# Kernel optimization log

Hardware: AMD Instinct MI355X
Metric: run time of the kernel (lower is better)

The kernel has to match this reference:

```python
import jax, jax.numpy as jnp
import numpy as np

N, E, IN, HID, H, G, CLS = 20000, 160000, 128, 96, 6, 512, 128
HD = H * HID  # heads * out_channels = 576
ARC_S = 30.0  # ArcFace scale (no margin at inference, no labels passed)


def _lin_params(key, fan_in, fan_out):
    k1, k2 = jax.random.split(key)
    lim = 1.0 / np.sqrt(fan_in)
    W = jax.random.uniform(k1, (fan_in, fan_out), minval=-lim, maxval=lim, dtype=jnp.float32)
    b = jax.random.uniform(k2, (fan_out,), minval=-lim, maxval=lim, dtype=jnp.float32)
    return W, b


def setup_inputs() -> dict:
    key = jax.random.key(0)
    ks = jax.random.split(key, 32)
    x = jax.random.normal(ks[0], (N, IN), dtype=jnp.float32)
    edge_index = jax.random.randint(ks[1], (2, E), 0, N, dtype=jnp.int64)
    batch = jnp.sort(jax.random.randint(ks[2], (N,), 0, G, dtype=jnp.int64))
    # conv1: IN -> HID (per-head dim HID, H heads)
    Wq1, bq1 = _lin_params(ks[3], IN, HD)
    Wk1, bk1 = _lin_params(ks[4], IN, HD)
    Wv1, bv1 = _lin_params(ks[5], IN, HD)
    Ws1, bs1 = _lin_params(ks[6], IN, HID)
    # convs 2..5 share shapes: HID -> HID, stacked on leading axis of 4
    def stack(fn_keys, fi, fo):
        Ws, bs = zip(*[_lin_params(k, fi, fo) for k in fn_keys])
        return jnp.stack(Ws), jnp.stack(bs)
    Wq_r, bq_r = stack(ks[7:11], HID, HD)
    Wk_r, bk_r = stack(ks[11:15], HID, HD)
    Wv_r, bv_r = stack(ks[15:19], HID, HD)
    Ws_r, bs_r = stack(ks[19:23], HID, HID)
    fc1_w, fc1_b = _lin_params(ks[23], HID, HID)
    fc2_w, fc2_b = _lin_params(ks[24], HID, HID)
    arc_w = jax.random.normal(ks[25], (CLS, HID), dtype=jnp.float32)
    return dict(x=x, edge_index=edge_index, batch=batch,
                Wq1=Wq1, bq1=bq1, Wk1=Wk1, bk1=bk1, Wv1=Wv1, bv1=bv1, Ws1=Ws1, bs1=bs1,
                Wq_r=Wq_r, bq_r=bq_r, Wk_r=Wk_r, bk_r=bk_r, Wv_r=Wv_r, bv_r=bv_r,
                Ws_r=Ws_r, bs_r=bs_r,
                fc1_w=fc1_w, fc1_b=fc1_b, fc2_w=fc2_w, fc2_b=fc2_b, arc_w=arc_w)


def transformer_conv(x, src, dst, Wq, bq, Wk, bk, Wv, bv, Ws, bs):
    n = x.shape[0]
    q = (x @ Wq + bq).reshape(n, H, HID)
    k = (x @ Wk + bk).reshape(n, H, HID)
    v = (x @ Wv + bv).reshape(n, H, HID)
    # edge-wise attention logits [E, H]
    alpha = jnp.einsum('ehd,ehd->eh', q[dst], k[src]) / jnp.sqrt(jnp.float32(HID))
    # segment softmax over incoming edges of each destination node
    m = jax.ops.segment_max(alpha, dst, num_segments=n)
    a = jnp.exp(alpha - m[dst])
    s = jax.ops.segment_sum(a, dst, num_segments=n)
    a = a / s[dst]
    out = jax.ops.segment_sum(a[:, :, None] * v[src], dst, num_segments=n)  # [n, H, HID]
    # concat=False -> mean over heads; root_weight skip connection
    return out.mean(axis=1) + x @ Ws + bs


def reference(x, edge_index, batch,
              Wq1, bq1, Wk1, bk1, Wv1, bv1, Ws1, bs1,
              Wq_r, bq_r, Wk_r, bk_r, Wv_r, bv_r, Ws_r, bs_r,
              fc1_w, fc1_b, fc2_w, fc2_b, arc_w):
    src, dst = edge_index[0], edge_index[1]
    h = jax.nn.relu(transformer_conv(x, src, dst, Wq1, bq1, Wk1, bk1, Wv1, bv1, Ws1, bs1))
    for i in range(4):  # gtconv2..gtconv5
        h = jax.nn.relu(transformer_conv(h, src, dst, Wq_r[i], bq_r[i], Wk_r[i], bk_r[i],
                                         Wv_r[i], bv_r[i], Ws_r[i], bs_r[i]))
    # global mean pool over graphs
    sums = jax.ops.segment_sum(h, batch, num_segments=G)
    cnt = jax.ops.segment_sum(jnp.ones((h.shape[0], 1), h.dtype), batch, num_segments=G)
    g = sums / jnp.maximum(cnt, 1.0)
    g = jax.nn.relu(g @ fc1_w + fc1_b)
    g = jax.nn.relu(g @ fc2_w + fc2_b)
    # ArcFace without labels: scaled cosine logits
    gn = g / (jnp.linalg.norm(g, axis=-1, keepdims=True) + 1e-12)
    wn = arc_w / (jnp.linalg.norm(arc_w, axis=-1, keepdims=True) + 1e-12)
    return ARC_S * (gn @ wn.T)
```

## Files before the change

### kernel.cpp

```cpp
#include <hip/hip_runtime.h>
#include <math.h>

#define N_NODES 20000
#define N_EDGES 160000
#define DIM_IN  128
#define HIDDEN  96
#define NH      6
#define HD      576
#define LDROW   704
#define KVF8LD  1152
#define NALL    1824
#define NGRAPH  512
#define NCLS    128
#define CHUNK   32
#define SLD     104
#define BSTR    112

typedef unsigned short ushort_t;
typedef unsigned char uchar_t;
typedef __attribute__((ext_vector_type(8))) short bf16x8;
typedef __attribute__((ext_vector_type(4))) float f32x4;
typedef __attribute__((ext_vector_type(2))) float f32x2;

static __device__ __forceinline__ ushort_t f2bf(float f) {
    unsigned int u = __float_as_uint(f);
    return (ushort_t)((u + 0x7fffu + ((u >> 16) & 1u)) >> 16);
}
static __device__ __forceinline__ float bfs(ushort_t u) { return __uint_as_float((unsigned int)u << 16); }
static __device__ __forceinline__ float bflo(unsigned int u) { return __uint_as_float(u << 16); }
static __device__ __forceinline__ float bfhi(unsigned int u) { return __uint_as_float(u & 0xffff0000u); }

#define PREP_CVT_BLOCKS 10000
#define PREP_DEG_BLOCKS 625
#define PREP_GB_BLOCKS  3
__global__ void k_prep(const float* __restrict__ x, ushort_t* __restrict__ xb,
                       const int* __restrict__ edst, int* __restrict__ deg,
                       const int* __restrict__ batch, int* __restrict__ gbound)
{
    int b = blockIdx.x;
    if (b < PREP_CVT_BLOCKS) {
        int i = b * 256 + threadIdx.x;
        if (i < N_NODES * DIM_IN) xb[i] = f2bf(x[i]);
    } else if (b < PREP_CVT_BLOCKS + PREP_DEG_BLOCKS) {
        int e = (b - PREP_CVT_BLOCKS) * 256 + threadIdx.x;
        if (e < N_EDGES) atomicAdd(&deg[edst[e]], 1);
    } else {
        int g = (b - PREP_CVT_BLOCKS - PREP_DEG_BLOCKS) * 256 + threadIdx.x;
        if (g <= NGRAPH) {
            int lo = 0, hi = N_NODES;
            while (lo < hi) {
                int mid = (lo + hi) >> 1;
                if (batch[mid] < g) lo = mid + 1; else hi = mid;
            }
            gbound[g] = lo;
        }
    }
}

__global__ void k_cvt_wT_all(
    const float* __restrict__ Wq1, const float* __restrict__ Wk1,
    const float* __restrict__ Wv1, const float* __restrict__ Ws1,
    const float* __restrict__ Wq_r, const float* __restrict__ Wk_r,
    const float* __restrict__ Wv_r, const float* __restrict__ Ws_r,
    ushort_t* __restrict__ Wb0, ushort_t* __restrict__ Wbr)
{
    const int L = blockIdx.y;
    const int K = (L == 0) ? DIM_IN : HIDDEN;
    int i = blockIdx.x * blockDim.x + threadIdx.x;
    if (i >= K * NALL) return;
    const float *Wq, *Wk, *Wv, *Ws; ushort_t* dst;
    if (L == 0) { Wq = Wq1; Wk = Wk1; Wv = Wv1; Ws = Ws1; dst = Wb0; }
    else {
        int j = L - 1;
        Wq = Wq_r + (size_t)j * HIDDEN * HD; Wk = Wk_r + (size_t)j * HIDDEN * HD;
        Wv = Wv_r + (size_t)j * HIDDEN * HD; Ws = Ws_r + (size_t)j * HIDDEN * HIDDEN;
        dst = Wbr + (size_t)j * HIDDEN * NALL;
    }
    int n = i / K, k = i - n * K;
    float v;
    if (n < 576)       v = Wq[(size_t)k * HD + n];
    else if (n < 1152) v = Wk[(size_t)k * HD + (n - 576)];
    else if (n < 1728) v = Wv[(size_t)k * HD + (n - 1152)];
    else               v = Ws[(size_t)k * HIDDEN + (n - 1728)];
    dst[i] = f2bf(v);
}

template<int KDIM>
__global__ __launch_bounds__(256) void gemm_qkvs_mfma(
    const ushort_t* __restrict__ A, int M,
    const ushort_t* __restrict__ WbT,
    const float* __restrict__ bq, const float* __restrict__ bk,
    const float* __restrict__ bv, const float* __restrict__ bs,
    ushort_t* __restrict__ kvqs, uchar_t* __restrict__ kvf8)
{
    constexpr int LDB = KDIM + 8;
    constexpr int K8  = KDIM >> 3;
    __shared__ __align__(16) ushort_t smem[128 * SLD];
    const int t    = threadIdx.x;
    const int lane = t & 63;
    const int w    = t >> 6;
    const int wm   = w & 1, wn = w >> 1;
    const int quad = lane >> 4;
    const int l16  = lane & 15;
    const int m0   = blockIdx.y * 128;
    const int rb   = blockIdx.x;
    const int n0   = rb * 96;

    for (int idx = t; idx < 96 * K8; idx += 256) {
        int c = idx / K8, kc = idx - c * K8;
        uint4 v = *(const uint4*)(WbT + (size_t)(n0 + c) * KDIM + kc * 8);
        *(uint4*)(&smem[c * LDB + kc * 8]) = v;
    }

    const ushort_t* Arow[4];
    #pragma unroll
    for (int i = 0; i < 4; i++) {
        int row = m0 + wm * 64 + i * 16 + l16;
        row = min(row, M - 1);
        Arow[i] = A + (size_t)row * KDIM + quad * 8;
    }
    __syncthreads();

    f32x4 acc[4][3] = {};
    #pragma unroll
    for (int ks = 0; ks < KDIM; ks += 32) {
        bf16x8 af[4], bfv[3];
        #pragma unroll
        for (int i = 0; i < 4; i++) af[i] = *(const bf16x8*)(Arow[i] + ks);
        #pragma unroll
        for (int j = 0; j < 3; j++)
            bfv[j] = *(const bf16x8*)(&smem[(wn * 48 + j * 16 + l16) * LDB + ks + quad * 8]);
        #pragma unroll
        for (int i = 0; i < 4; i++)
            #pragma unroll
            for (int j = 0; j < 3; j++)
                acc[i][j] = __builtin_amdgcn_mfma_f32_16x16x32_bf16(af[i], bfv[j], acc[i][j], 0, 0, 0);
    }

    int region; const float* biasp;
    if (rb < 6)       { region = 0; biasp = bq; }
    else if (rb < 12) { region = 1; biasp = bk; }
    else if (rb < 18) { region = 2; biasp = bv; }
    else              { region = 3; biasp = bs; }
    const int colbase = (region == 3) ? 0 : (rb - region * 6) * 96;
    float bj[3];
    #pragma unroll
    for (int j = 0; j < 3; j++) bj[j] = biasp[colbase + wn * 48 + j * 16 + l16];

    __syncthreads();

    if (region == 1 || region == 2) {
        uchar_t* bstage = (uchar_t*)smem;
        #pragma unroll
        for (int i = 0; i < 4; i++) {
            #pragma unroll
            for (int r = 0; r < 4; r++) {
                int row = wm * 64 + i * 16 + quad * 4 + r;
                #pragma unroll
                for (int j = 0; j < 3; j++) {
                    float v = acc[i][j][r] + bj[j];
                    int pk = __builtin_amdgcn_cvt_pk_fp8_f32(v, v, 0, false);
                    bstage[row * BSTR + wn * 48 + j * 16 + l16] = (uchar_t)(pk & 0xff);
                }
            }
        }
        __syncthreads();
        const int c0 = (rb - 6) * 96;
        for (int idx = t; idx < 128 * 6; idx += 256) {
            int r = idx / 6, v4 = idx - r * 6;
            int row = m0 + r;
            if (row < M)
                *(uint4*)(kvf8 + (size_t)row * KVF8LD + c0 + v4 * 16) =
                    *(const uint4*)(bstage + r * BSTR + v4 * 16);
        }
    } else {
        int dstoff = (region == 0) ? n0 : 576;
        #pragma unroll
        for (int i = 0; i < 4; i++) {
            #pragma unroll
            for (int r = 0; r < 4; r++) {
                int row = wm * 64 + i * 16 + quad * 4 + r;
                #pragma unroll
                for (int j = 0; j < 3; j++)
                    smem[row * SLD + wn * 48 + j * 16 + l16] = f2bf(acc[i][j][r] + bj[j]);
            }
        }
        __syncthreads();
        for (int idx = t; idx < 128 * 12; idx += 256) {
            int r = idx / 12, v = idx - r * 12;
            int row = m0 + r;
            if (row < M)
                *(uint4*)(kvqs + (size_t)row * LDROW + dstoff + v * 8) =
                    *(const uint4*)(&smem[r * SLD + v * 8]);
        }
    }
}

__global__ __launch_bounds__(1024) void k_scan(const int* __restrict__ deg,
                                               int* __restrict__ row_ptr,
                                               int* __restrict__ cursor)
{
    __shared__ int part[1024];
    int t = threadIdx.x;
    const int chunk = (N_NODES + 1023) / 1024;
    int b = t * chunk;
    int s = 0;
    for (int i = 0; i < chunk; i++)
        if (b + i < N_NODES) s += deg[b + i];
    part[t] = s;
    __syncthreads();
    for (int o = 1; o < 1024; o <<= 1) {
        int v = (t >= o) ? part[t - o] : 0;
        __syncthreads();
        part[t] += v;
        __syncthreads();
    }
    int run = part[t] - s;
    for (int i = 0; i < chunk; i++) {
        if (b + i < N_NODES) {
            row_ptr[b + i] = run;
            cursor[b + i]  = run;
            run += deg[b + i];
        }
    }
    if (t == 1023) row_ptr[N_NODES] = part[1023];
}

__global__ void k_scatter(const int* __restrict__ esrc, const int* __restrict__ edst,
                          int* __restrict__ cursor, int* __restrict__ csrc)
{
    int e = blockIdx.x * blockDim.x + threadIdx.x;
    if (e < N_EDGES) {
        int pos = atomicAdd(&cursor[edst[e]], 1);
        csrc[pos] = esrc[e];
    }
}

__global__ __launch_bounds__(64) void node_attn(
    const ushort_t* __restrict__ kvqs, const uchar_t* __restrict__ kvf8,
    const int* __restrict__ row_ptr, const int* __restrict__ csrc,
    ushort_t* __restrict__ hb)
{
    const int n    = blockIdx.x;
    const int lane = threadIdx.x;

    __shared__ float QA[HD];
    __shared__ float wbuf[CHUNK * NH];
    __shared__ int   srcs[CHUNK];
    __shared__ float mh[NH], lh[NH], scl[NH], linv[NH];

    const int beg = row_ptr[n], end = row_ptr[n + 1];
    const ushort_t* qk = kvqs + (size_t)n * LDROW;

    {
        uint4 v = *(const uint4*)(qk + lane * 8);
        unsigned int uu[4] = {v.x, v.y, v.z, v.w};
        #pragma unroll
        for (int j = 0; j < 4; j++) {
            QA[lane * 8 + 2 * j]     = bflo(uu[j]);
            QA[lane * 8 + 2 * j + 1] = bfhi(uu[j]);
        }
        if (lane < 8) {
            uint4 v2 = *(const uint4*)(qk + (64 + lane) * 8);
            unsigned int uu2[4] = {v2.x, v2.y, v2.z, v2.w};
            #pragma unroll
            for (int j = 0; j < 4; j++) {
                QA[(64 + lane) * 8 + 2 * j]     = bflo(uu2[j]);
                QA[(64 + lane) * 8 + 2 * j + 1] = bfhi(uu2[j]);
            }
        }
    }
    if (lane < NH) { mh[lane] = -1e30f; lh[lane] = 0.f; }

    const int sub = lane >> 5;
    const int h32 = lane & 31;
    const int g   = h32 >> 2;
    const int gg  = (g < 6) ? g : 0;
    const int qr  = h32 & 3;
    const int hh  = lane >> 3;
    const int j8  = lane & 7;
    const uchar_t* vb = kvf8 + 576 + ((hh < 6) ? hh : 0) * HIDDEN + j8 * 12;

    float acc[12];
    #pragma unroll
    for (int d = 0; d < 12; d++) acc[d] = 0.f;
    const float qa = 0.10206207261596577f;

    __syncthreads();

    for (int cb = beg; cb < end; cb += CHUNK) {
        const int c = min(CHUNK, end - cb);
        if (lane < c) srcs[lane] = csrc[cb + lane];
        __syncthreads();

        for (int eb = 0; eb < c; eb += 8) {
            unsigned int kb[4][6];
            #pragma unroll
            for (int j = 0; j < 4; j++) {
                int e = eb + 2 * j + sub;
                int src = srcs[(e < c) ? e : 0];
                const uchar_t* kp = kvf8 + (size_t)src * KVF8LD + gg * HIDDEN + qr * 24;
                uint2 a0 = *(const uint2*)(kp);
                uint2 a1 = *(const uint2*)(kp + 8);
                uint2 a2 = *(const uint2*)(kp + 16);
                kb[j][0] = a0.x; kb[j][1] = a0.y;
                kb[j][2] = a1.x; kb[j][3] = a1.y;
                kb[j][4] = a2.x; kb[j][5] = a2.y;
            }
            const float* qb = &QA[gg * HIDDEN + qr * 24];
            #pragma unroll
            for (int j = 0; j < 4; j++) {
                int e = eb + 2 * j + sub;
                bool act = (e < c) && (g < 6);
                float p = 0.f;
                #pragma unroll
                for (int k2 = 0; k2 < 6; k2++) {
                    f32x2 lo = __builtin_amdgcn_cvt_pk_f32_fp8(kb[j][k2], false);
                    f32x2 hi = __builtin_amdgcn_cvt_pk_f32_fp8(kb[j][k2], true);
                    p += lo[0] * qb[4 * k2]     + lo[1] * qb[4 * k2 + 1]
                       + hi[0] * qb[4 * k2 + 2] + hi[1] * qb[4 * k2 + 3];
                }
                p += __shfl_xor(p, 1, 64);
                p += __shfl_xor(p, 2, 64);
                if (act && qr == 0) wbuf[e * NH + g] = p * qa;
            }
        }
        __syncthreads();

        #pragma unroll
        for (int s = 0; s < 3; s++) {
            int h = 2 * s + sub;
            float logit = (h32 < c) ? wbuf[h32 * NH + h] : -1e30f;
            float cm = logit;
            #pragma unroll
            for (int o = 16; o; o >>= 1) cm = fmaxf(cm, __shfl_xor(cm, o, 32));
            cm = fmaxf(cm, mh[h]);
            float wv = (h32 < c) ? __expf(logit - cm) : 0.f;
            if (h32 < c) wbuf[h32 * NH + h] = wv;
            float lp = wv;
            #pragma unroll
            for (int o = 16; o; o >>= 1) lp += __shfl_xor(lp, o, 32);
            if (h32 == 0) {
                float sc = __expf(mh[h] - cm);
                scl[h] = sc;
                lh[h] = lh[h] * sc + lp;
                mh[h] = cm;
            }
        }
        __syncthreads();

        if (lane < 48) {
            float sc = scl[hh];
            #pragma unroll
            for (int d = 0; d < 12; d++) acc[d] *= sc;
            int e = 0;
            for (; e + 4 <= c; e += 4) {
                unsigned int r[4][3];
                #pragma unroll
                for (int j = 0; j < 4; j++) {
                    const uchar_t* p = vb + (size_t)srcs[e + j] * KVF8LD;
                    r[j][0] = *(const unsigned int*)(p);
                    r[j][1] = *(const unsigned int*)(p + 4);
                    r[j][2] = *(const unsigned int*)(p + 8);
                }
                #pragma unroll
                for (int j = 0; j < 4; j++) {
                    float w0 = wbuf[(e + j) * NH + hh];
                    #pragma unroll
                    for (int k = 0; k < 3; k++) {
                        f32x2 lo = __builtin_amdgcn_cvt_pk_f32_fp8(r[j][k], false);
                        f32x2 hi = __builtin_amdgcn_cvt_pk_f32_fp8(r[j][k], true);
                        acc[4 * k]     += w0 * lo[0];
                        acc[4 * k + 1] += w0 * lo[1];
                        acc[4 * k + 2] += w0 * hi[0];
                        acc[4 * k + 3] += w0 * hi[1];
                    }
                }
            }
            for (; e < c; e++) {
                const uchar_t* p0 = vb + (size_t)srcs[e] * KVF8LD;
                float w0 = wbuf[e * NH + hh];
                #pragma unroll
                for (int k = 0; k < 3; k++) {
                    unsigned int r = *(const unsigned int*)(p0 + 4 * k);
                    f32x2 lo = __builtin_amdgcn_cvt_pk_f32_fp8(r, false);
                    f32x2 hi = __builtin_amdgcn_cvt_pk_f32_fp8(r, true);
                    acc[4 * k]     += w0 * lo[0];
                    acc[4 * k + 1] += w0 * lo[1];
                    acc[4 * k + 2] += w0 * hi[0];
                    acc[4 * k + 3] += w0 * hi[1];
                }
            }
        }
        __syncthreads();
    }

    if (lane < NH) linv[lane] = (lh[lane] > 0.f) ? 1.0f / lh[lane] : 0.f;
    __syncthreads();
    if (lane < 48) {
        float li = linv[hh];
        #pragma unroll
        for (int d = 0; d < 12; d++)
            QA[hh * HIDDEN + j8 * 12 + d] = acc[d] * li;
    }
    __syncthreads();

    {
        int d = lane;
        float s = (QA[d] + QA[HIDDEN + d] + QA[2 * HIDDEN + d] +
                   QA[3 * HIDDEN + d] + QA[4 * HIDDEN + d] + QA[5 * HIDDEN + d])
                  * (1.0f / 6.0f);
        s += bfs(qk[576 + d]);
        s = fmaxf(s, 0.0f);
        hb[n * HIDDEN + d] = f2bf(s);
        if (lane < 32) {
            int d2 = 64 + lane;
            float s2 = (QA[d2] + QA[HIDDEN + d2] + QA[2 * HIDDEN + d2] +
                        QA[3 * HIDDEN + d2] + QA[4 * HIDDEN + d2] + QA[5 * HIDDEN + d2])
                       * (1.0f / 6.0f);
            s2 += bfs(qk[576 + d2]);
            s2 = fmaxf(s2, 0.0f);
            hb[n * HIDDEN + d2] = f2bf(s2);
        }
    }
}

__global__ __launch_bounds__(128) void k_head(
    const ushort_t* __restrict__ hb, const int* __restrict__ gbound,
    const float* __restrict__ fc1w, const float* __restrict__ fc1b,
    const float* __restrict__ fc2w, const float* __restrict__ fc2b,
    const float* __restrict__ arcw, float* __restrict__ out)
{
    int g = blockIdx.x, t = threadIdx.x;
    __shared__ float v0[HIDDEN], v1[HIDDEN], v2[HIDDEN];
    __shared__ float gnorm;
    const int s0 = gbound[g], s1 = gbound[g + 1];
    float cnt = fmaxf((float)(s1 - s0), 1.0f);
    if (t < HIDDEN) {
        float s = 0.f;
        for (int n = s0; n < s1; n++) s += bfs(hb[(size_t)n * HIDDEN + t]);
        v0[t] = s / cnt;
    }
    __syncthreads();
    if (t < HIDDEN) {
        float s = fc1b[t];
        for (int k = 0; k < HIDDEN; k++) s += v0[k] * fc1w[k * HIDDEN + t];
        v1[t] = fmaxf(s, 0.f);
    }
    __syncthreads();
    if (t < HIDDEN) {
        float s = fc2b[t];
        for (int k = 0; k < HIDDEN; k++) s += v1[k] * fc2w[k * HIDDEN + t];
        v2[t] = fmaxf(s, 0.f);
    }
    __syncthreads();
    if (t == 0) {
        float s = 0.f;
        for (int k = 0; k < HIDDEN; k++) s += v2[k] * v2[k];
        gnorm = sqrtf(s) + 1e-12f;
    }
    __syncthreads();
    if (t < NCLS) {
        float dot = 0.f, wn = 0.f;
        const float* wr = arcw + (size_t)t * HIDDEN;
        for (int k = 0; k < HIDDEN; k++) {
            float w = wr[k];
            dot += w * v2[k];
            wn  += w * w;
        }
        out[g * NCLS + t] = 30.0f * dot / (gnorm * (sqrtf(wn) + 1e-12f));
    }
}

extern "C" void kernel_launch(void* const* d_in, const int* in_sizes, int n_in,
                              void* d_out, int out_size, void* d_ws, size_t ws_size,
                              hipStream_t stream)
{
    (void)in_sizes; (void)n_in; (void)out_size; (void)ws_size;

    const float* x     = (const float*)d_in[0];
    const int*   ei    = (const int*)d_in[1];
    const int*   batch = (const int*)d_in[2];
    const float* Wq1 = (const float*)d_in[3];  const float* bq1 = (const float*)d_in[4];
    const float* Wk1 = (const float*)d_in[5];  const float* bk1 = (const float*)d_in[6];
    const float* Wv1 = (const float*)d_in[7];  const float* bv1 = (const float*)d_in[8];
    const float* Ws1 = (const float*)d_in[9];  const float* bs1 = (const float*)d_in[10];
    const float* Wq_r = (const float*)d_in[11]; const float* bq_r = (const float*)d_in[12];
    const float* Wk_r = (const float*)d_in[13]; const float* bk_r = (const float*)d_in[14];
    const float* Wv_r = (const float*)d_in[15]; const float* bv_r = (const float*)d_in[16];
    const float* Ws_r = (const float*)d_in[17]; const float* bs_r = (const float*)d_in[18];
    const float* fc1w = (const float*)d_in[19]; const float* fc1b = (const float*)d_in[20];
    const float* fc2w = (const float*)d_in[21]; const float* fc2b = (const float*)d_in[22];
    const float* arcw = (const float*)d_in[23];
    float* out = (float*)d_out;

    const int* esrc = ei;
    const int* edst = ei + N_EDGES;

    char* base = (char*)d_ws;
    size_t off = 0;
    auto alloc = [&](size_t bytes) -> void* {
        off = (off + 255) & ~(size_t)255;
        void* p = base + off;
        off += bytes;
        return p;
    };
    ushort_t* kvqs = (ushort_t*)alloc((size_t)N_NODES * LDROW * 2);
    uchar_t*  kvf8 = (uchar_t*)alloc((size_t)N_NODES * KVF8LD);
    ushort_t* xb  = (ushort_t*)alloc((size_t)N_NODES * DIM_IN * 2);
    ushort_t* hb0 = (ushort_t*)alloc((size_t)N_NODES * HIDDEN * 2);
    ushort_t* hb1 = (ushort_t*)alloc((size_t)N_NODES * HIDDEN * 2);
    ushort_t* Wb0 = (ushort_t*)alloc((size_t)DIM_IN * NALL * 2);
    ushort_t* Wbr = (ushort_t*)alloc((size_t)4 * HIDDEN * NALL * 2);
    int*   deg     = (int*)alloc(N_NODES * 4);
    int*   row_ptr = (int*)alloc((N_NODES + 1) * 4);
    int*   cursor  = (int*)alloc(N_NODES * 4);
    int*   csrc    = (int*)alloc(N_EDGES * 4);
    int*   gbound  = (int*)alloc((NGRAPH + 1) * 4);

    hipMemsetAsync(deg, 0, N_NODES * 4, stream);
    k_prep<<<PREP_CVT_BLOCKS + PREP_DEG_BLOCKS + PREP_GB_BLOCKS, 256, 0, stream>>>(
        x, xb, edst, deg, batch, gbound);
    {
        dim3 gw((DIM_IN * NALL + 255) / 256, 5);
        k_cvt_wT_all<<<gw, 256, 0, stream>>>(Wq1, Wk1, Wv1, Ws1,
                                             Wq_r, Wk_r, Wv_r, Ws_r, Wb0, Wbr);
    }
    k_scan<<<1, 1024, 0, stream>>>(deg, row_ptr, cursor);
    k_scatter<<<(N_EDGES + 255) / 256, 256, 0, stream>>>(esrc, edst, cursor, csrc);

    const ushort_t* Ain = xb;
    ushort_t* hbcur = hb0;
    for (int L = 0; L < 5; L++) {
        const ushort_t* Wb = (L == 0) ? Wb0 : (Wbr + (size_t)(L - 1) * HIDDEN * NALL);
        const float *bq, *bk, *bv, *bs;
        if (L == 0) { bq = bq1; bk = bk1; bv = bv1; bs = bs1; }
        else {
            int i = L - 1;
            bq = bq_r + (size_t)i * HD; bk = bk_r + (size_t)i * HD;
            bv = bv_r + (size_t)i * HD; bs = bs_r + (size_t)i * HIDDEN;
        }
        dim3 g(19, (N_NODES + 127) / 128);
        if (L == 0)
            gemm_qkvs_mfma<DIM_IN><<<g, 256, 0, stream>>>(Ain, N_NODES, Wb,
                                                          bq, bk, bv, bs, kvqs, kvf8);
        else
            gemm_qkvs_mfma<HIDDEN><<<g, 256, 0, stream>>>(Ain, N_NODES, Wb,
                                                          bq, bk, bv, bs, kvqs, kvf8);
        node_attn<<<N_NODES, 64, 0, stream>>>(kvqs, kvf8, row_ptr, csrc, hbcur);
        Ain = hbcur;
        hbcur = (hbcur == hb0) ? hb1 : hb0;
    }

    k_head<<<NGRAPH, 128, 0, stream>>>(hbcur == hb0 ? hb1 : hb0, gbound,
                                       fc1w, fc1b, fc2w, fc2b, arcw, out);
}
```

Measured before the change: 532.7 us.

## Split attention into edge-parallel logit kernel and per-node aggregation kernel

Attention logit computation moves out of the per-node kernel into a new edge-parallel kernel that reads Q (bf16) and K (fp8) per edge and writes logits to a global buffer. The node kernel then only loads the precomputed logits and does softmax plus V aggregation. The aim is to spread the dot-product work evenly across edges instead of serialising it per node with degree imbalance. In exchange it adds an extra launch per layer, a global round trip of E×6 floats, and repeated per-edge Q reads instead of one Q load per node.

```diff
diff --git a/kernel.cpp b/kernel.cpp
--- a/kernel.cpp
+++ b/kernel.cpp
@@ -227,56 +227,98 @@
 }
 
 __global__ void k_scatter(const int* __restrict__ esrc, const int* __restrict__ edst,
-                          int* __restrict__ cursor, int* __restrict__ csrc)
+                          int* __restrict__ cursor, int* __restrict__ csrc,
+                          int* __restrict__ cdst)
 {
     int e = blockIdx.x * blockDim.x + threadIdx.x;
     if (e < N_EDGES) {
-        int pos = atomicAdd(&cursor[edst[e]], 1);
+        int d = edst[e];
+        int pos = atomicAdd(&cursor[d], 1);
         csrc[pos] = esrc[e];
-    }
-}
-
-__global__ __launch_bounds__(64) void node_attn(
+        cdst[pos] = d;
+    }
+}
+
+#define ELOG_EPW    16
+#define ELOG_BLOCKS (N_EDGES / (ELOG_EPW * 4))
+__global__ __launch_bounds__(256) void k_edge_logits(
+    const ushort_t* __restrict__ kvqs, const uchar_t* __restrict__ kvf8,
+    const int* __restrict__ csrc, const int* __restrict__ cdst,
+    float* __restrict__ alphag)
+{
+    const int wid  = (blockIdx.x * 256 + threadIdx.x) >> 6;
+    const int lane = threadIdx.x & 63;
+    const int sub  = lane >> 5;
+    const int h32  = lane & 31;
+    const int g    = h32 >> 2;
+    const int gg   = (g < 6) ? g : 0;
+    const int qr   = h32 & 3;
+    const float qa = 0.10206207261596577f;
+
+    const int base0 = wid * ELOG_EPW;
+
+    for (int off = 0; off < ELOG_EPW; off += 4) {
+        const int base = base0 + off;
+        unsigned int kb[2][6];
+        unsigned int qb[2][12];
+        #pragma unroll
+        for (int j = 0; j < 2; j++) {
+            int e  = base + 2 * j + sub;
+            int ec = min(e, N_EDGES - 1);
+            int src = csrc[ec], dst = cdst[ec];
+            const uchar_t* kp = kvf8 + (size_t)src * KVF8LD + gg * HIDDEN + qr * 24;
+            uint2 a0 = *(const uint2*)(kp);
+            uint2 a1 = *(const uint2*)(kp + 8);
+            uint2 a2 = *(const uint2*)(kp + 16);
+            kb[j][0] = a0.x; kb[j][1] = a0.y; kb[j][2] = a1.x;
+            kb[j][3] = a1.y; kb[j][4] = a2.x; kb[j][5] = a2.y;
+            const ushort_t* qp = kvqs + (size_t)dst * LDROW + gg * HIDDEN + qr * 24;
+            uint4 q0 = *(const uint4*)(qp);
+            uint4 q1 = *(const uint4*)(qp + 8);
+            uint4 q2 = *(const uint4*)(qp + 16);
+            qb[j][0] = q0.x; qb[j][1] = q0.y; qb[j][2]  = q0.z; qb[j][3]  = q0.w;
+            qb[j][4] = q1.x; qb[j][5] = q1.y; qb[j][6]  = q1.z; qb[j][7]  = q1.w;
+            qb[j][8] = q2.x; qb[j][9] = q2.y; qb[j][10] = q2.z; qb[j][11] = q2.w;
+        }
+        #pragma unroll
+        for (int j = 0; j < 2; j++) {
+            int e = base + 2 * j + sub;
+            float p = 0.f;
+            #pragma unroll
+            for (int k2 = 0; k2 < 6; k2++) {
+                f32x2 lo = __builtin_amdgcn_cvt_pk_f32_fp8(kb[j][k2], false);
+                f32x2 hi = __builtin_amdgcn_cvt_pk_f32_fp8(kb[j][k2], true);
+                p += lo[0] * bflo(qb[j][2 * k2])     + lo[1] * bfhi(qb[j][2 * k2])
+                   + hi[0] * bflo(qb[j][2 * k2 + 1]) + hi[1] * bfhi(qb[j][2 * k2 + 1]);
+            }
+            p += __shfl_xor(p, 1, 64);
+            p += __shfl_xor(p, 2, 64);
+            if (e < N_EDGES && g < 6 && qr == 0)
+                alphag[(size_t)e * NH + g] = p * qa;
+        }
+    }
+}
+
+__global__ __launch_bounds__(64) void k_node_agg(
     const ushort_t* __restrict__ kvqs, const uchar_t* __restrict__ kvf8,
     const int* __restrict__ row_ptr, const int* __restrict__ csrc,
-    ushort_t* __restrict__ hb)
+    const float* __restrict__ alphag, ushort_t* __restrict__ hb)
 {
     const int n    = blockIdx.x;
     const int lane = threadIdx.x;
 
-    __shared__ float QA[HD];
     __shared__ float wbuf[CHUNK * NH];
     __shared__ int   srcs[CHUNK];
     __shared__ float mh[NH], lh[NH], scl[NH], linv[NH];
+    __shared__ float arr[HD];
 
     const int beg = row_ptr[n], end = row_ptr[n + 1];
     const ushort_t* qk = kvqs + (size_t)n * LDROW;
 
-    {
-        uint4 v = *(const uint4*)(qk + lane * 8);
-        unsigned int uu[4] = {v.x, v.y, v.z, v.w};
-        #pragma unroll
-        for (int j = 0; j < 4; j++) {
-            QA[lane * 8 + 2 * j]     = bflo(uu[j]);
-            QA[lane * 8 + 2 * j + 1] = bfhi(uu[j]);
-        }
-        if (lane < 8) {
-            uint4 v2 = *(const uint4*)(qk + (64 + lane) * 8);
-            unsigned int uu2[4] = {v2.x, v2.y, v2.z, v2.w};
-            #pragma unroll
-            for (int j = 0; j < 4; j++) {
-                QA[(64 + lane) * 8 + 2 * j]     = bflo(uu2[j]);
-                QA[(64 + lane) * 8 + 2 * j + 1] = bfhi(uu2[j]);
-            }
-        }
-    }
     if (lane < NH) { mh[lane] = -1e30f; lh[lane] = 0.f; }
 
     const int sub = lane >> 5;
     const int h32 = lane & 31;
-    const int g   = h32 >> 2;
-    const int gg  = (g < 6) ? g : 0;
-    const int qr  = h32 & 3;
     const int hh  = lane >> 3;
     const int j8  = lane & 7;
     const uchar_t* vb = kvf8 + 576 + ((hh < 6) ? hh : 0) * HIDDEN + j8 * 12;
@@ -284,47 +326,14 @@
     float acc[12];
     #pragma unroll
     for (int d = 0; d < 12; d++) acc[d] = 0.f;
-    const float qa = 0.10206207261596577f;
 
     __syncthreads();
 
     for (int cb = beg; cb < end; cb += CHUNK) {
         const int c = min(CHUNK, end - cb);
         if (lane < c) srcs[lane] = csrc[cb + lane];
-        __syncthreads();
-
-        for (int eb = 0; eb < c; eb += 8) {
-            unsigned int kb[4][6];
-            #pragma unroll
-            for (int j = 0; j < 4; j++) {
-                int e = eb + 2 * j + sub;
-                int src = srcs[(e < c) ? e : 0];
-                const uchar_t* kp = kvf8 + (size_t)src * KVF8LD + gg * HIDDEN + qr * 24;
-                uint2 a0 = *(const uint2*)(kp);
-                uint2 a1 = *(const uint2*)(kp + 8);
-                uint2 a2 = *(const uint2*)(kp + 16);
-                kb[j][0] = a0.x; kb[j][1] = a0.y;
-                kb[j][2] = a1.x; kb[j][3] = a1.y;
-                kb[j][4] = a2.x; kb[j][5] = a2.y;
-            }
-            const float* qb = &QA[gg * HIDDEN + qr * 24];
-            #pragma unroll
-            for (int j = 0; j < 4; j++) {
-                int e = eb + 2 * j + sub;
-                bool act = (e < c) && (g < 6);
-                float p = 0.f;
-                #pragma unroll
-                for (int k2 = 0; k2 < 6; k2++) {
-                    f32x2 lo = __builtin_amdgcn_cvt_pk_f32_fp8(kb[j][k2], false);
-                    f32x2 hi = __builtin_amdgcn_cvt_pk_f32_fp8(kb[j][k2], true);
-                    p += lo[0] * qb[4 * k2]     + lo[1] * qb[4 * k2 + 1]
-                       + hi[0] * qb[4 * k2 + 2] + hi[1] * qb[4 * k2 + 3];
-                }
-                p += __shfl_xor(p, 1, 64);
-                p += __shfl_xor(p, 2, 64);
-                if (act && qr == 0) wbuf[e * NH + g] = p * qa;
-            }
-        }
+        for (int i = lane; i < c * NH; i += 64)
+            wbuf[i] = alphag[(size_t)cb * NH + i];
         __syncthreads();
 
         #pragma unroll
@@ -401,22 +410,22 @@
         float li = linv[hh];
         #pragma unroll
         for (int d = 0; d < 12; d++)
-            QA[hh * HIDDEN + j8 * 12 + d] = acc[d] * li;
+            arr[hh * HIDDEN + j8 * 12 + d] = acc[d] * li;
     }
     __syncthreads();
 
     {
         int d = lane;
-        float s = (QA[d] + QA[HIDDEN + d] + QA[2 * HIDDEN + d] +
-                   QA[3 * HIDDEN + d] + QA[4 * HIDDEN + d] + QA[5 * HIDDEN + d])
+        float s = (arr[d] + arr[HIDDEN + d] + arr[2 * HIDDEN + d] +
+                   arr[3 * HIDDEN + d] + arr[4 * HIDDEN + d] + arr[5 * HIDDEN + d])
                   * (1.0f / 6.0f);
         s += bfs(qk[576 + d]);
         s = fmaxf(s, 0.0f);
         hb[n * HIDDEN + d] = f2bf(s);
         if (lane < 32) {
             int d2 = 64 + lane;
-            float s2 = (QA[d2] + QA[HIDDEN + d2] + QA[2 * HIDDEN + d2] +
-                        QA[3 * HIDDEN + d2] + QA[4 * HIDDEN + d2] + QA[5 * HIDDEN + d2])
+            float s2 = (arr[d2] + arr[HIDDEN + d2] + arr[2 * HIDDEN + d2] +
+                        arr[3 * HIDDEN + d2] + arr[4 * HIDDEN + d2] + arr[5 * HIDDEN + d2])
                        * (1.0f / 6.0f);
             s2 += bfs(qk[576 + d2]);
             s2 = fmaxf(s2, 0.0f);
@@ -512,10 +521,12 @@
     ushort_t* hb1 = (ushort_t*)alloc((size_t)N_NODES * HIDDEN * 2);
     ushort_t* Wb0 = (ushort_t*)alloc((size_t)DIM_IN * NALL * 2);
     ushort_t* Wbr = (ushort_t*)alloc((size_t)4 * HIDDEN * NALL * 2);
+    float* alphag  = (float*)alloc((size_t)N_EDGES * NH * 4);
     int*   deg     = (int*)alloc(N_NODES * 4);
     int*   row_ptr = (int*)alloc((N_NODES + 1) * 4);
     int*   cursor  = (int*)alloc(N_NODES * 4);
     int*   csrc    = (int*)alloc(N_EDGES * 4);
+    int*   cdst    = (int*)alloc(N_EDGES * 4);
     int*   gbound  = (int*)alloc((NGRAPH + 1) * 4);
 
     hipMemsetAsync(deg, 0, N_NODES * 4, stream);
@@ -527,7 +538,7 @@
                                              Wq_r, Wk_r, Wv_r, Ws_r, Wb0, Wbr);
     }
     k_scan<<<1, 1024, 0, stream>>>(deg, row_ptr, cursor);
-    k_scatter<<<(N_EDGES + 255) / 256, 256, 0, stream>>>(esrc, edst, cursor, csrc);
+    k_scatter<<<(N_EDGES + 255) / 256, 256, 0, stream>>>(esrc, edst, cursor, csrc, cdst);
 
     const ushort_t* Ain = xb;
     ushort_t* hbcur = hb0;
@@ -547,7 +558,8 @@
         else
             gemm_qkvs_mfma<HIDDEN><<<g, 256, 0, stream>>>(Ain, N_NODES, Wb,
                                                           bq, bk, bv, bs, kvqs, kvf8);
-        node_attn<<<N_NODES, 64, 0, stream>>>(kvqs, kvf8, row_ptr, csrc, hbcur);
+        k_edge_logits<<<ELOG_BLOCKS, 256, 0, stream>>>(kvqs, kvf8, csrc, cdst, alphag);
+        k_node_agg<<<N_NODES, 64, 0, stream>>>(kvqs, kvf8, row_ptr, csrc, alphag, hbcur);
         Ain = hbcur;
         hbcur = (hbcur == hb0) ? hb1 : hb0;
     }
```

New measurement: 561.0 us. 5.3% more time.
